# Kernel optimization log

Hardware: AMD Instinct MI355X
Metric: run time of the kernel (lower is better)

The kernel has to match this reference:

```python
import jax, jax.numpy as jnp
import numpy as np

# Fixed architecture constants (match init_kwargs)
L = 4        # num_layers
E = 4        # embed_dim (forced: embedding rows are 4-bit patch vectors)
H = 512      # hidden_dim
NH = 8       # num_heads
HD = H // NH # head_dim = 64
FF = 1024    # feedforward_dim
S = 1024     # seq_len (num patches)
B = 4        # batch
NT = 17      # num_tokens (16 patterns + mask token)
MRP = 32     # max_relative_positions
EPS = 1e-5


def _layernorm(x, g, b):
    m = x.mean(-1, keepdims=True)
    v = x.var(-1, keepdims=True)  # torch LayerNorm uses biased variance
    return (x - m) / jnp.sqrt(v + EPS) * g + b


def setup_inputs() -> dict:
    key = jax.random.key(0)
    ks = jax.random.split(key, 16)
    patches = jax.random.randint(ks[0], (B, S), 0, 16)
    mask = jax.random.bernoulli(ks[1], 0.15, (B, S))
    # Frozen embedding table: rows 0..15 = binary 4-vectors, row 16 = all 2s (mask token)
    pat = np.array([[a, b, c, d] for a in range(2) for b in range(2)
                    for c in range(2) for d in range(2)], dtype=np.float32)
    emb = np.zeros((NT, E), np.float32)
    emb[:16] = pat
    emb[16] = 2.0
    emb_table = jnp.array(emb)

    def gn(k, shape, s=0.02):
        return jax.random.normal(k, shape, jnp.float32) * s

    return {
        'patches': patches,
        'mask': mask,
        'emb_table': emb_table,
        'Wi': gn(ks[2], (L, E, H)), 'bi': jnp.zeros((L, H)),
        'Wqkv': gn(ks[3], (L, H, 3 * H)), 'bqkv': jnp.zeros((L, 3 * H)),
        'Wo': gn(ks[4], (L, H, E)), 'bo': jnp.zeros((L, E)),
        'g1': jnp.ones((L, H)), 'b1n': jnp.zeros((L, H)),
        'Wf1': gn(ks[5], (L, E, FF)), 'bf1': jnp.zeros((L, FF)),
        'Wf2': gn(ks[6], (L, FF, E)), 'bf2': jnp.zeros((L, E)),
        'g2': jnp.ones((L, E)), 'b2n': jnp.zeros((L, E)),
        'relemb': jax.random.normal(ks[7], (L, 2 * MRP - 1, HD), jnp.float32),
        'Wout': gn(ks[8], (E, NT)), 'bout': jnp.zeros((NT,)),
    }


def reference(patches, mask, emb_table, Wi, bi, Wqkv, bqkv, Wo, bo,
              g1, b1n, Wf1, bf1, Wf2, bf2, g2, b2n, relemb, Wout, bout):
    # Embedding lookup + mask-token substitution
    x = emb_table[patches]                                # (B,S,E)
    x = jnp.where(mask[..., None], emb_table[-1], x)

    r = jnp.arange(S)
    relpos = jnp.clip(r[:, None] - r[None, :] + MRP - 1, 0, 2 * MRP - 2)  # (S,S)
    # The original's nested-loop mask-build reduces exactly to:
    #   score[b,q,k] += -inf  iff  mask[b,k] and q != k
    neg = jnp.where(mask[:, None, :] & (r[:, None] != r[None, :]),
                    -jnp.inf, 0.0)                        # (B,S,S)

    scale = 1.0 / np.sqrt(HD)
    for l in range(L):
        bias = relemb[l].sum(-1)[relpos]                  # (S,S) rel-pos bias
        xp = x @ Wi[l] + bi[l]                            # (B,S,H)
        xn = _layernorm(xp, g1[l], b1n[l])
        qkv = (xn @ Wqkv[l] + bqkv[l]).reshape(B, S, 3, NH, HD)
        q, k, v = qkv[:, :, 0], qkv[:, :, 1], qkv[:, :, 2]
        sc = jnp.einsum('bqhd,bkhd->bhqk', q, k) * scale + bias + neg[:, None]
        p = jax.nn.softmax(sc, axis=-1)                   # (B,NH,S,S)
        ao = jnp.einsum('bhqk,bkhd->bqhd', p, v).reshape(B, S, H)
        x = x + ao @ Wo[l] + bo[l]                        # residual 1 (embed dim E)
        ff = jax.nn.relu(_layernorm(x, g2[l], b2n[l]) @ Wf1[l] + bf1[l]) @ Wf2[l] + bf2[l]
        x = x + ff                                        # residual 2
    return x @ Wout + bout                                # (B,S,NT) logits
```

## Files before the change

kernel.cpp:

```cpp
#include <hip/hip_runtime.h>
#include <hip/hip_bf16.h>
#include <math.h>

#define B_ 4
#define S_ 1024
#define H_ 512
#define NH_ 8
#define HD_ 64
#define FF_ 1024
#define E_ 4
#define L_ 4
#define NT_ 17
#define BS_ 4096
#define EPS_ 1e-5f
#define L2E_ 1.4426950408889634f
#define SCL_ 0.18033688011112042f
#define KSPLIT_ 4

typedef __attribute__((ext_vector_type(8))) short short8;
typedef __attribute__((ext_vector_type(16))) float f32x16;
typedef float float4u __attribute__((ext_vector_type(4), aligned(4)));

__device__ inline ushort bf16_rne(float f) {
  unsigned u = __builtin_bit_cast(unsigned, f);
  u += 0x7FFFu + ((u >> 16) & 1u);
  return (ushort)(u >> 16);
}
__device__ inline unsigned pk_bf16(float a, float b) {
  return (unsigned)bf16_rne(a) | ((unsigned)bf16_rne(b) << 16);
}
__device__ inline unsigned pk2(float a, float b) {
  unsigned ua = __builtin_bit_cast(unsigned, a) + 0x8000u;
  unsigned ub = __builtin_bit_cast(unsigned, b) + 0x8000u;
  return __builtin_amdgcn_perm(ub, ua, 0x07060302u);
}
__device__ inline float ubf2f(ushort u) {
  return __builtin_bit_cast(float, ((unsigned)u) << 16);
}


__global__ __launch_bounds__(256) void k_pre(const int* __restrict__ patches,
                                             const int* __restrict__ mask,
                                             const float* __restrict__ emb,
                                             const float* __restrict__ relemb,
                                             const float* __restrict__ W,
                                             const float* __restrict__ Wi,
                                             const float* __restrict__ bi,
                                             const float* __restrict__ g1,
                                             const float* __restrict__ b1n,
                                             float* __restrict__ x,
                                             float* __restrict__ T,
                                             float* __restrict__ negT,
                                             ushort* __restrict__ Wt,
                                             ushort* __restrict__ xnbf) {
  __shared__ ushort Tr[64][72];
  int bid = blockIdx.x, t = threadIdx.x;
  if (bid < 768) {
    int l = bid / 192, rem = bid % 192;
    int k0 = (rem / 24) * 64, n0 = (rem % 24) * 64;
    const float* src = W + (size_t)l * 512 * 1536;
    int row = t >> 4, c4 = (t & 15) * 4;
#pragma unroll
    for (int rr = 0; rr < 4; rr++) {
      int k = rr * 16 + row;
      float4 v = *(const float4*)(src + (size_t)(k0 + k) * 1536 + n0 + c4);
      Tr[c4 + 0][k] = bf16_rne(v.x);
      Tr[c4 + 1][k] = bf16_rne(v.y);
      Tr[c4 + 2][k] = bf16_rne(v.z);
      Tr[c4 + 3][k] = bf16_rne(v.w);
    }
    __syncthreads();
    int nrow = t >> 2, kc = (t & 3) * 16;
    ushort* dst = Wt + ((size_t)(l * 1536 + n0 + nrow)) * 512 + k0 + kc;
    *(uint4*)dst = *(uint4*)&Tr[nrow][kc];
    *(uint4*)(dst + 8) = *(uint4*)&Tr[nrow][kc + 8];
  } else if (bid < 817) {
    int gid = (bid - 768) * 256 + t;
    if (gid < BS_) {
      int mk = mask[gid];
      int row = mk ? (NT_ - 1) : patches[gid];
      ((float4*)x)[gid] = ((const float4*)emb)[row];
      negT[gid] = mk ? -1e30f : 0.f;
    } else {
      int idx = gid - BS_;
      if (idx < L_ * 2112) {
        int l = idx / 2112, j = idx - l * 2112;
        int c = 1086 - j;
        c = c < 0 ? 0 : (c > 62 ? 62 : c);
        const float* src = relemb + (size_t)(l * 63 + c) * 64;
        float s = 0.f;
#pragma unroll
        for (int d = 0; d < 64; d++) s += src[d];
        T[idx] = s * L2E_;
      }
    }
  } else {
    int token = (bid - 817) * 4 + (t >> 6);
    int lane = t & 63;
    int mk = mask[token];
    int row = mk ? (NT_ - 1) : patches[token];
    float4 e = ((const float4*)emb)[row];
    float xp[8];
    float s = 0.f, qs = 0.f;
#pragma unroll
    for (int k = 0; k < 8; k++) {
      int jj = 64 * k + lane;
      float v = bi[jj] + e.x * Wi[jj] + e.y * Wi[H_ + jj] + e.z * Wi[2 * H_ + jj] + e.w * Wi[3 * H_ + jj];
      xp[k] = v; s += v; qs += v * v;
    }
#pragma unroll
    for (int o = 1; o < 64; o <<= 1) { s += __shfl_xor(s, o); qs += __shfl_xor(qs, o); }
    float mean = s * (1.f / (float)H_);
    float var = qs * (1.f / (float)H_) - mean * mean;
    float rs = rsqrtf(var + EPS_);
#pragma unroll
    for (int k = 0; k < 8; k++) {
      int jj = 64 * k + lane;
      xnbf[token * H_ + jj] = bf16_rne((xp[k] - mean) * rs * g1[jj] + b1n[jj]);
    }
  }
}

__global__ __launch_bounds__(512, 4) void k_qkv(const ushort* __restrict__ A,
                                                const ushort* __restrict__ Wt,
                                                const float* __restrict__ bias,
                                                ushort* __restrict__ qf,
                                                ushort* __restrict__ kf,
                                                ushort* __restrict__ vf) {
  __shared__ ushort At[2][128][72];
  __shared__ ushort Bt[2][128][72];
  int t = threadIdx.x;
  int n0 = blockIdx.x * 128, m0 = blockIdx.y * 128;
  bool tr = (n0 < 1024);
  int w = t >> 6, lq = t & 31, hh = (t >> 5) & 1;
  int wm = (w & 1) * 64, wn = (w >> 1) * 32;
  f32x16 acc[2];
#pragma unroll
  for (int mt = 0; mt < 2; mt++)
#pragma unroll
    for (int i = 0; i < 16; i++) acc[mt][i] = 0.f;

  uint4 ar[2], br[2];

#define QLOADREGS(k0_)                                                         \
  {                                                                            \
    _Pragma("unroll") for (int j = 0; j < 2; j++) {                            \
      int idl = 512 * j + t;                                                   \
      int row = idl >> 3, u = idl & 7;                                         \
      ar[j] = *(const uint4*)(A + (size_t)(m0 + row) * 512 + (k0_) + u * 8);   \
      br[j] = *(const uint4*)(Wt + (size_t)(n0 + row) * 512 + (k0_) + u * 8);  \
    }                                                                          \
  }
#define QWRITELDS(buf_)                                                        \
  {                                                                            \
    _Pragma("unroll") for (int j = 0; j < 2; j++) {                            \
      int idl = 512 * j + t;                                                   \
      int row = idl >> 3, u = idl & 7;                                         \
      *(uint4*)&At[buf_][row][u * 8] = ar[j];                                  \
      *(uint4*)&Bt[buf_][row][u * 8] = br[j];                                  \
    }                                                                          \
  }

  QLOADREGS(0);
  QWRITELDS(0);
  __syncthreads();

  for (int it = 0; it < 8; it++) {
    int buf = it & 1;
    if (it < 7) { QLOADREGS((it + 1) * 64); }
#pragma unroll
    for (int kc = 0; kc < 4; kc++) {
      short8 af[2], bf;
#pragma unroll
      for (int mt = 0; mt < 2; mt++) af[mt] = *(const short8*)&At[buf][wm + mt * 32 + lq][kc * 16 + hh * 8];
      bf = *(const short8*)&Bt[buf][wn + lq][kc * 16 + hh * 8];
#pragma unroll
      for (int mt = 0; mt < 2; mt++) {
        if (tr)
          acc[mt] = __builtin_amdgcn_mfma_f32_32x32x16_bf16(bf, af[mt], acc[mt], 0, 0, 0);
        else
          acc[mt] = __builtin_amdgcn_mfma_f32_32x32x16_bf16(af[mt], bf, acc[mt], 0, 0, 0);
      }
    }
    if (it < 7) {
      QWRITELDS(buf ^ 1);
      __syncthreads();
    }
  }
#undef QLOADREGS
#undef QWRITELDS

  if (tr) {
#pragma unroll
    for (int mt = 0; mt < 2; mt++) {
      int token = m0 + wm + mt * 32 + lq;
      int bb = token >> 10, sr = token & 1023;
      int qt = sr >> 5, lqp = sr & 31;
      int nn = n0 + wn;
      int nloc = (nn < 512) ? nn : nn - 512;
      ushort* dst = (nn < 512) ? qf : kf;
      int hd = nloc >> 6;
      int bh = bb * 8 + hd;
      size_t fragbase = ((size_t)(bh * 32 + qt)) * 4 * 512;
#pragma unroll
      for (int rg = 0; rg < 4; rg++) {
        int nbase = nn + rg * 8 + hh * 4;
        float4 bv = *(const float4*)(bias + nbase);
        float v0 = acc[mt][rg * 4 + 0] + bv.x;
        float v1 = acc[mt][rg * 4 + 1] + bv.y;
        float v2 = acc[mt][rg * 4 + 2] + bv.z;
        float v3 = acc[mt][rg * 4 + 3] + bv.w;
        int d0 = (nloc & 63) + rg * 8 + hh * 4;
        size_t addr = fragbase + (size_t)(d0 >> 4) * 512 +
                      (size_t)(((d0 >> 3) & 1) * 32 + lqp) * 8 + (d0 & 7);
        *(uint2*)(dst + addr) = make_uint2(pk_bf16(v0, v1), pk_bf16(v2, v3));
      }
    }
  } else {
    int n = n0 + wn + lq;
    int nloc = n - 1024;
    int hd = nloc >> 6, d = nloc & 63;
    float bb_ = bias[n];
#pragma unroll
    for (int mt = 0; mt < 2; mt++) {
#pragma unroll
      for (int rg = 0; rg < 4; rg++) {
        int tb = m0 + wm + mt * 32 + rg * 8 + hh * 4;
        int bb = tb >> 10, sr = tb & 1023;
        int bh = bb * 8 + hd;
        float v0 = acc[mt][rg * 4 + 0] + bb_;
        float v1 = acc[mt][rg * 4 + 1] + bb_;
        float v2 = acc[mt][rg * 4 + 2] + bb_;
        float v3 = acc[mt][rg * 4 + 3] + bb_;
        size_t addr = ((size_t)((bh * 2 + (d >> 5)) * 64 + (sr >> 4))) * 512 +
                      (size_t)(((sr >> 3) & 1) * 32 + (d & 31)) * 8 + (sr & 7);
        *(uint2*)(vf + addr) = make_uint2(pk_bf16(v0, v1), pk_bf16(v2, v3));
      }
    }
  }
}

__global__ __launch_bounds__(256, 4) void k_attn(const ushort* __restrict__ qf,
                                                 const ushort* __restrict__ kf,
                                                 const ushort* __restrict__ vf,
                                                 const float* __restrict__ Tl,
                                                 const float* __restrict__ negT,
                                                 const float* __restrict__ Wol,
                                                 float* __restrict__ AOp,
                                                 float* __restrict__ lpart) {
  __shared__ ushort Pt[4][32][72];
  int t = threadIdx.x;
  int w = t >> 6, lane = t & 63;
  int lq = lane & 31, hh = lane >> 5;
  int id = blockIdx.x;
  int bh = id & 31;
  int slot = id >> 5;
  int qtg = slot & 7, j = slot >> 3;
  int b = bh >> 3, head = bh & 7;
  int qt = qtg * 4 + w;
  int q = qt * 32 + lq;
  int kstart = j * 256;

  const ushort* qbase = qf + ((size_t)(bh * 32 + qt)) * 2048 + lane * 8;
  short8 Qf[4];
#pragma unroll
  for (int c = 0; c < 4; c++) Qf[c] = *(const short8*)(qbase + c * 512);

  float Tlo = Tl[1086];
  float Thi = Tl[1024];

  float l_run = 0.f;
  f32x16 Ot[2];
#pragma unroll
  for (int dt = 0; dt < 2; dt++)
#pragma unroll
    for (int i = 0; i < 16; i++) Ot[dt][i] = 0.f;

  for (int it = 0; it < 4; it++) {
    int k0 = kstart + it * 64;
#pragma unroll
    for (int st = 0; st < 2; st++) {
      const ushort* kb = kf + ((size_t)(bh * 32 + (k0 >> 5) + st)) * 2048 + lane * 8;
      short8 Kb[4];
#pragma unroll
      for (int c = 0; c < 4; c++) Kb[c] = *(const short8*)(kb + c * 512);
      f32x16 sa;
#pragma unroll
      for (int i = 0; i < 16; i++) sa[i] = 0.f;
#pragma unroll
      for (int c = 0; c < 4; c++)
        sa = __builtin_amdgcn_mfma_f32_32x32x16_bf16(Kb[c], Qf[c], sa, 0, 0, 0);
      int kt0 = k0 + st * 32;
      int delta = kt0 - qt * 32;
      if (delta >= 64 || delta <= -64) {
        float bconst = (delta >= 64) ? Tlo : Thi;
#pragma unroll
        for (int rg = 0; rg < 4; rg++) {
          int krun = kt0 + rg * 8 + hh * 4;
          float4 nv = *(const float4*)(negT + b * S_ + krun);
          float p0 = exp2f(fmaf(sa[rg * 4 + 0], SCL_, bconst + nv.x));
          float p1 = exp2f(fmaf(sa[rg * 4 + 1], SCL_, bconst + nv.y));
          float p2 = exp2f(fmaf(sa[rg * 4 + 2], SCL_, bconst + nv.z));
          float p3 = exp2f(fmaf(sa[rg * 4 + 3], SCL_, bconst + nv.w));
          l_run += (p0 + p1) + (p2 + p3);
          *(uint2*)&Pt[w][lq][st * 32 + rg * 8 + hh * 4] = make_uint2(pk2(p0, p1), pk2(p2, p3));
        }
      } else {
#pragma unroll
        for (int rg = 0; rg < 4; rg++) {
          int krun = kt0 + rg * 8 + hh * 4;
          float4u bv = *(const float4u*)(Tl + (krun - q + 31 + 1024));
          float4 nv = *(const float4*)(negT + b * S_ + krun);
          float pp[4];
#pragma unroll
          for (int i = 0; i < 4; i++) {
            float nvi = (i == 0) ? nv.x : (i == 1) ? nv.y : (i == 2) ? nv.z : nv.w;
            float t0 = (krun + i == q) ? bv[i] : (bv[i] + nvi);
            pp[i] = exp2f(fmaf(sa[rg * 4 + i], SCL_, t0));
            l_run += pp[i];
          }
          *(uint2*)&Pt[w][lq][st * 32 + rg * 8 + hh * 4] = make_uint2(pk2(pp[0], pp[1]), pk2(pp[2], pp[3]));
        }
      }
    }
    short8 Pf[4];
#pragma unroll
    for (int c = 0; c < 4; c++) Pf[c] = *(const short8*)&Pt[w][lq][c * 16 + hh * 8];
#pragma unroll
    for (int dt = 0; dt < 2; dt++) {
      const ushort* vbp = vf + ((size_t)((bh * 2 + dt) * 64 + (k0 >> 4))) * 512 + lane * 8;
      short8 Vb[4];
#pragma unroll
      for (int c = 0; c < 4; c++) Vb[c] = *(const short8*)(vbp + c * 512);
#pragma unroll
      for (int c = 0; c < 4; c++)
        Ot[dt] = __builtin_amdgcn_mfma_f32_32x32x16_bf16(Vb[c], Pf[c], Ot[dt], 0, 0, 0);
    }
  }
  const float* woh = Wol + head * 64 * 4;
  float pe0 = 0.f, pe1 = 0.f, pe2 = 0.f, pe3 = 0.f;
#pragma unroll
  for (int dt = 0; dt < 2; dt++)
#pragma unroll
    for (int rg = 0; rg < 4; rg++)
#pragma unroll
      for (int i = 0; i < 4; i++) {
        int d = dt * 32 + rg * 8 + hh * 4 + i;
        float4 wv = *(const float4*)(woh + d * 4);
        float o = Ot[dt][rg * 4 + i];
        pe0 = fmaf(o, wv.x, pe0);
        pe1 = fmaf(o, wv.y, pe1);
        pe2 = fmaf(o, wv.z, pe2);
        pe3 = fmaf(o, wv.w, pe3);
      }
  pe0 += __shfl_xor(pe0, 32);
  pe1 += __shfl_xor(pe1, 32);
  pe2 += __shfl_xor(pe2, 32);
  pe3 += __shfl_xor(pe3, 32);
  float l_tot = l_run + __shfl_xor(l_run, 32);
  if (hh == 0) {
    float* ao = AOp + (size_t)j * (BS_ * NH_ * 4) + ((size_t)(b * S_ + q) * NH_ + head) * 4;
    *(float4*)ao = make_float4(pe0, pe1, pe2, pe3);
    lpart[((size_t)j * 32 + bh) * S_ + q] = l_tot;
  }
}

__global__ __launch_bounds__(256) void k_resffn(const float* __restrict__ AOp,
                                                const float* __restrict__ lpart,
                                                const float* __restrict__ bo,
                                                const float* __restrict__ g2,
                                                const float* __restrict__ b2n,
                                                const float* __restrict__ Wf1,
                                                const float* __restrict__ bf1,
                                                const float* __restrict__ Wf2,
                                                const float* __restrict__ bf2,
                                                float* __restrict__ x,
                                                const float* __restrict__ Wi,
                                                const float* __restrict__ bi,
                                                const float* __restrict__ g1,
                                                const float* __restrict__ b1n,
                                                ushort* __restrict__ xnbf,
                                                int doinln,
                                                const float* __restrict__ Wout,
                                                const float* __restrict__ bout,
                                                float* __restrict__ out,
                                                int dofinal) {
  int tok = blockIdx.x * 4 + (threadIdx.x >> 6);
  int lane = threadIdx.x & 63;
  int b = tok >> 10, qq = tok & 1023;
  int h = lane & 7;
  int lidx = (b * 8 + h) * 1024 + qq;
  float ls = lpart[lidx] + lpart[lidx + 32768] + lpart[lidx + 65536] + lpart[lidx + 98304];
  float inv = 1.f / ls;
  size_t abase = ((size_t)tok * 8 + h) * 4;
  float4 v0 = *(const float4*)(AOp + abase);
  float4 v1 = *(const float4*)(AOp + abase + 131072);
  float4 v2 = *(const float4*)(AOp + abase + 262144);
  float4 v3 = *(const float4*)(AOp + abase + 393216);
  float r0 = (v0.x + v1.x + v2.x + v3.x) * inv;
  float r1 = (v0.y + v1.y + v2.y + v3.y) * inv;
  float r2 = (v0.z + v1.z + v2.z + v3.z) * inv;
  float r3 = (v0.w + v1.w + v2.w + v3.w) * inv;
#pragma unroll
  for (int o = 1; o < 8; o <<= 1) {
    r0 += __shfl_xor(r0, o); r1 += __shfl_xor(r1, o);
    r2 += __shfl_xor(r2, o); r3 += __shfl_xor(r3, o);
  }
  float4 xo = *(const float4*)&x[tok * 4];
  float x0 = xo.x + r0 + bo[0];
  float x1 = xo.y + r1 + bo[1];
  float x2 = xo.z + r2 + bo[2];
  float x3 = xo.w + r3 + bo[3];
  float mn = 0.25f * (x0 + x1 + x2 + x3);
  float d0 = x0 - mn, d1 = x1 - mn, d2 = x2 - mn, d3 = x3 - mn;
  float var = 0.25f * (d0 * d0 + d1 * d1 + d2 * d2 + d3 * d3);
  float rs = rsqrtf(var + EPS_);
  float l0 = d0 * rs * g2[0] + b2n[0];
  float l1 = d1 * rs * g2[1] + b2n[1];
  float l2 = d2 * rs * g2[2] + b2n[2];
  float l3 = d3 * rs * g2[3] + b2n[3];
  float f0 = 0, f1 = 0, f2 = 0, f3 = 0;
#pragma unroll
  for (int f4 = 0; f4 < FF_ / 64; f4++) {
    int f = lane + f4 * 64;
    float hh = bf1[f] + l0 * Wf1[f] + l1 * Wf1[FF_ + f] + l2 * Wf1[2 * FF_ + f] + l3 * Wf1[3 * FF_ + f];
    hh = fmaxf(hh, 0.f);
    float4 w2 = *(const float4*)&Wf2[f * 4];
    f0 += hh * w2.x; f1 += hh * w2.y; f2 += hh * w2.z; f3 += hh * w2.w;
  }
#pragma unroll
  for (int o = 1; o < 64; o <<= 1) {
    f0 += __shfl_xor(f0, o); f1 += __shfl_xor(f1, o);
    f2 += __shfl_xor(f2, o); f3 += __shfl_xor(f3, o);
  }
  x0 += f0 + bf2[0]; x1 += f1 + bf2[1]; x2 += f2 + bf2[2]; x3 += f3 + bf2[3];
  if (dofinal) {
    if (lane < NT_)
      out[tok * NT_ + lane] = bout[lane] + x0 * Wout[lane] + x1 * Wout[NT_ + lane] +
                              x2 * Wout[2 * NT_ + lane] + x3 * Wout[3 * NT_ + lane];
    return;
  }
  if (lane == 0) *(float4*)&x[tok * 4] = make_float4(x0, x1, x2, x3);
  if (doinln) {
    float xp[8];
    float s = 0.f, qs = 0.f;
#pragma unroll
    for (int k = 0; k < 8; k++) {
      int jj = 64 * k + lane;
      float v = bi[jj] + x0 * Wi[jj] + x1 * Wi[H_ + jj] + x2 * Wi[2 * H_ + jj] + x3 * Wi[3 * H_ + jj];
      xp[k] = v;
      s += v;
      qs += v * v;
    }
#pragma unroll
    for (int o = 1; o < 64; o <<= 1) {
      s += __shfl_xor(s, o);
      qs += __shfl_xor(qs, o);
    }
    float mean = s * (1.f / (float)H_);
    float var1 = qs * (1.f / (float)H_) - mean * mean;
    float rs1 = rsqrtf(var1 + EPS_);
#pragma unroll
    for (int k = 0; k < 8; k++) {
      int jj = 64 * k + lane;
      float v = (xp[k] - mean) * rs1 * g1[jj] + b1n[jj];
      xnbf[tok * H_ + jj] = bf16_rne(v);
    }
  }
}

extern "C" void kernel_launch(void* const* d_in, const int* in_sizes, int n_in,
                              void* d_out, int out_size, void* d_ws, size_t ws_size,
                              hipStream_t stream) {
  const int* patches = (const int*)d_in[0];
  const int* mask = (const int*)d_in[1];
  const float* emb = (const float*)d_in[2];
  const float* Wi = (const float*)d_in[3];
  const float* bi = (const float*)d_in[4];
  const float* Wqkv = (const float*)d_in[5];
  const float* bqkv = (const float*)d_in[6];
  const float* Wo = (const float*)d_in[7];
  const float* bo = (const float*)d_in[8];
  const float* g1 = (const float*)d_in[9];
  const float* b1n = (const float*)d_in[10];
  const float* Wf1 = (const float*)d_in[11];
  const float* bf1 = (const float*)d_in[12];
  const float* Wf2 = (const float*)d_in[13];
  const float* bf2 = (const float*)d_in[14];
  const float* g2 = (const float*)d_in[15];
  const float* b2n = (const float*)d_in[16];
  const float* relemb = (const float*)d_in[17];
  const float* Wout = (const float*)d_in[18];
  const float* bout = (const float*)d_in[19];
  float* out = (float*)d_out;

  char* p = (char*)d_ws;
  float* x = (float*)p;          p += (size_t)BS_ * 4 * 4;
  float* T = (float*)p;          p += (size_t)L_ * 2112 * 4;
  float* negT = (float*)p;       p += (size_t)BS_ * 4;
  float* AOp = (float*)p;        p += (size_t)KSPLIT_ * BS_ * NH_ * 4 * 4;
  float* lpart = (float*)p;      p += (size_t)KSPLIT_ * 32 * 1024 * 4;
  ushort* xnbf = (ushort*)p;     p += (size_t)BS_ * H_ * 2;
  ushort* Wt = (ushort*)p;       p += (size_t)L_ * 1536 * 512 * 2;
  ushort* qf = (ushort*)p;       p += (size_t)32 * 1024 * 64 * 2;
  ushort* kf = (ushort*)p;       p += (size_t)32 * 1024 * 64 * 2;
  ushort* vf = (ushort*)p;       p += (size_t)32 * 64 * 1024 * 2;

  k_pre<<<dim3(1841), dim3(256), 0, stream>>>(patches, mask, emb, relemb, Wqkv,
                                              Wi, bi, g1, b1n, x, T, negT, Wt, xnbf);
  for (int l = 0; l < L_; l++) {
    k_qkv<<<dim3(12, 32), dim3(512), 0, stream>>>(xnbf, Wt + (size_t)l * 1536 * 512,
                                                  bqkv + l * 3 * H_, qf, kf, vf);
    k_attn<<<dim3(1024), dim3(256), 0, stream>>>(qf, kf, vf, T + l * 2112, negT,
                                                 Wo + l * H_ * E_, AOp, lpart);
    int nl = l + 1;
    k_resffn<<<dim3(1024), dim3(256), 0, stream>>>(
        AOp, lpart, bo + l * E_, g2 + l * E_, b2n + l * E_,
        Wf1 + l * E_ * FF_, bf1 + l * FF_, Wf2 + l * FF_ * E_, bf2 + l * E_, x,
        Wi + nl * E_ * H_, bi + nl * H_, g1 + nl * H_, b1n + nl * H_, xnbf,
        (l < L_ - 1) ? 1 : 0, Wout, bout, out, (l == L_ - 1) ? 1 : 0);
  }
}
```

Baseline: 299.2 us.

## Stage K/V tiles in LDS for attention and cache FFN weights in LDS

In the attention kernel, the four waves of a block now cooperatively load each 64-key K and V tile into shared memory and then read their MFMA operands from LDS, instead of each wave fetching the same tiles from global memory. Block barriers are added around each tile. The residual/FFN kernel copies Wf1, bf1 and Wf2 (about 36 KB) into shared memory per block before the FFN loop and gets a 4-blocks-per-SM launch bound. The aim is to cut redundant global/L2 traffic, but this adds barriers without double buffering in attention and a large per-block LDS fill in a kernel that handles only four tokens per block.

Result: faster. 286.7 us (median of 2 runs) (-4.2%).

```diff
diff --git a/kernel.cpp b/kernel.cpp
--- a/kernel.cpp
+++ b/kernel.cpp
@@ -248,6 +248,8 @@
                                                  const float* __restrict__ Wol,
                                                  float* __restrict__ AOp,
                                                  float* __restrict__ lpart) {
+  __shared__ ushort Kl[2][2048];
+  __shared__ ushort Vl[2][2048];
   __shared__ ushort Pt[4][32][72];
   int t = threadIdx.x;
   int w = t >> 6, lane = t & 63;
@@ -278,12 +280,22 @@
 
   for (int it = 0; it < 4; it++) {
     int k0 = kstart + it * 64;
+    {
+      const uint4* ks0 = (const uint4*)(kf + ((size_t)(bh * 32 + (k0 >> 5) + 0)) * 2048);
+      const uint4* ks1 = (const uint4*)(kf + ((size_t)(bh * 32 + (k0 >> 5) + 1)) * 2048);
+      const uint4* vs0 = (const uint4*)(vf + ((size_t)((bh * 2 + 0) * 64 + (k0 >> 4))) * 512);
+      const uint4* vs1 = (const uint4*)(vf + ((size_t)((bh * 2 + 1) * 64 + (k0 >> 4))) * 512);
+      ((uint4*)Kl[0])[t] = ks0[t];
+      ((uint4*)Kl[1])[t] = ks1[t];
+      ((uint4*)Vl[0])[t] = vs0[t];
+      ((uint4*)Vl[1])[t] = vs1[t];
+    }
+    __syncthreads();
 #pragma unroll
     for (int st = 0; st < 2; st++) {
-      const ushort* kb = kf + ((size_t)(bh * 32 + (k0 >> 5) + st)) * 2048 + lane * 8;
       short8 Kb[4];
 #pragma unroll
-      for (int c = 0; c < 4; c++) Kb[c] = *(const short8*)(kb + c * 512);
+      for (int c = 0; c < 4; c++) Kb[c] = *(const short8*)&Kl[st][lane * 8 + c * 512];
       f32x16 sa;
 #pragma unroll
       for (int i = 0; i < 16; i++) sa[i] = 0.f;
@@ -328,14 +340,14 @@
     for (int c = 0; c < 4; c++) Pf[c] = *(const short8*)&Pt[w][lq][c * 16 + hh * 8];
 #pragma unroll
     for (int dt = 0; dt < 2; dt++) {
-      const ushort* vbp = vf + ((size_t)((bh * 2 + dt) * 64 + (k0 >> 4))) * 512 + lane * 8;
       short8 Vb[4];
 #pragma unroll
-      for (int c = 0; c < 4; c++) Vb[c] = *(const short8*)(vbp + c * 512);
+      for (int c = 0; c < 4; c++) Vb[c] = *(const short8*)&Vl[dt][lane * 8 + c * 512];
 #pragma unroll
       for (int c = 0; c < 4; c++)
         Ot[dt] = __builtin_amdgcn_mfma_f32_32x32x16_bf16(Vb[c], Pf[c], Ot[dt], 0, 0, 0);
     }
+    __syncthreads();
   }
   const float* woh = Wol + head * 64 * 4;
   float pe0 = 0.f, pe1 = 0.f, pe2 = 0.f, pe3 = 0.f;
@@ -365,7 +377,7 @@
   }
 }
 
-__global__ __launch_bounds__(256) void k_resffn(const float* __restrict__ AOp,
+__global__ __launch_bounds__(256, 4) void k_resffn(const float* __restrict__ AOp,
                                                 const float* __restrict__ lpart,
                                                 const float* __restrict__ bo,
                                                 const float* __restrict__ g2,
@@ -385,8 +397,18 @@
                                                 const float* __restrict__ bout,
                                                 float* __restrict__ out,
                                                 int dofinal) {
-  int tok = blockIdx.x * 4 + (threadIdx.x >> 6);
-  int lane = threadIdx.x & 63;
+  __shared__ float Wf1s[4096];
+  __shared__ float bf1s[1024];
+  __shared__ float Wf2s[4096];
+  int t = threadIdx.x;
+#pragma unroll
+  for (int i = 0; i < 4; i++) ((float4*)Wf1s)[i * 256 + t] = ((const float4*)Wf1)[i * 256 + t];
+  ((float4*)bf1s)[t] = ((const float4*)bf1)[t];
+#pragma unroll
+  for (int i = 0; i < 4; i++) ((float4*)Wf2s)[i * 256 + t] = ((const float4*)Wf2)[i * 256 + t];
+
+  int tok = blockIdx.x * 4 + (t >> 6);
+  int lane = t & 63;
   int b = tok >> 10, qq = tok & 1023;
   int h = lane & 7;
   int lidx = (b * 8 + h) * 1024 + qq;
@@ -419,13 +441,14 @@
   float l1 = d1 * rs * g2[1] + b2n[1];
   float l2 = d2 * rs * g2[2] + b2n[2];
   float l3 = d3 * rs * g2[3] + b2n[3];
+  __syncthreads();
   float f0 = 0, f1 = 0, f2 = 0, f3 = 0;
 #pragma unroll
   for (int f4 = 0; f4 < FF_ / 64; f4++) {
     int f = lane + f4 * 64;
-    float hh = bf1[f] + l0 * Wf1[f] + l1 * Wf1[FF_ + f] + l2 * Wf1[2 * FF_ + f] + l3 * Wf1[3 * FF_ + f];
+    float hh = bf1s[f] + l0 * Wf1s[f] + l1 * Wf1s[FF_ + f] + l2 * Wf1s[2 * FF_ + f] + l3 * Wf1s[3 * FF_ + f];
     hh = fmaxf(hh, 0.f);
-    float4 w2 = *(const float4*)&Wf2[f * 4];
+    float4 w2 = *(const float4*)&Wf2s[f * 4];
     f0 += hh * w2.x; f1 += hh * w2.y; f2 += hh * w2.z; f3 += hh * w2.w;
   }
 #pragma unroll
```
